# Kernel tuning notes

Hardware: AMD Instinct MI355X
Metric: run time of the kernel (lower is better)

Reference implementation:

```python
import jax, jax.numpy as jnp
import numpy as np

N = 4096      # batch size (PK-sampled)
D = 1024      # feature dim
K = 4         # instances per identity
NUM_IDS = N // K


def setup_inputs() -> dict:
    key = jax.random.key(0)
    inputs = jax.random.normal(key, (N, D), dtype=jnp.float32)
    # PK-structured labels: NUM_IDS identities, K instances each.
    targets = jnp.repeat(jnp.arange(NUM_IDS, dtype=jnp.int32), K)
    # Flags alternate within each identity -> every (same/diff id) x (same/diff flag)
    # combination is non-empty for every anchor row.
    flags = jnp.tile(jnp.array([0, 1, 0, 1], dtype=jnp.int32), N // 4)
    epoch = 10  # unused by the loss, kept for signature fidelity
    return {"inputs": inputs, "targets": targets, "flags": flags, "epoch": epoch}


def reference(inputs, targets, flags, epoch):
    # Pairwise Euclidean distances: ||a||^2 + ||b||^2 - 2 a.b, clamped + sqrt.
    sq = jnp.sum(inputs * inputs, axis=1, keepdims=True)          # [n,1]
    dist = sq + sq.T - 2.0 * (inputs @ inputs.T)                   # [n,n]
    dist = jnp.sqrt(jnp.clip(dist, 1e-12, None))

    same_id = targets[:, None] == targets[None, :]                 # mask_1
    same_fl = flags[:, None] == flags[None, :]                     # mask_2
    m_same_hp = same_id & same_fl
    m_same_hn = (~same_id) & same_fl
    m_dif_hp = same_id & (~same_fl)
    m_dif_hn = (~same_id) & (~same_fl)

    NEG = jnp.asarray(-jnp.inf, dist.dtype)
    POS = jnp.asarray(jnp.inf, dist.dtype)
    dist_same_ap = jnp.max(jnp.where(m_same_hp, dist, NEG), axis=1)
    dist_same_an = jnp.min(jnp.where(m_same_hn, dist, POS), axis=1)
    dist_dif_ap = jnp.max(jnp.where(m_dif_hp, dist, NEG), axis=1)
    dist_dif_an = jnp.min(jnp.where(m_dif_hn, dist, POS), axis=1)

    # torch: first index in the FULL row equal to the masked min (exact equality)
    same_min_idx = jnp.argmax(dist == dist_same_an[:, None], axis=1)  # [n]
    dif_min_idx = jnp.argmax(dist == dist_dif_an[:, None], axis=1)    # [n]
    dist_dif_neg = dist[same_min_idx, dif_min_idx]                    # [n]

    relu = jax.nn.relu
    # MarginRankingLoss(x1, x2, y=1) = mean(relu(x2 - x1 + margin))
    loss_same = jnp.mean(relu(dist_same_ap - dist_same_an + 0.8))
    loss_dif = jnp.mean(relu(dist_dif_ap - dist_dif_an + 0.5))
    loss_neg = jnp.mean(relu(dist_same_ap - dist_dif_neg + 0.3))
    return loss_same + loss_dif + loss_neg
```

## Files before the change

### kernel.cpp

```cpp
#include <hip/hip_runtime.h>

#define NROWS 4096
#define DIM   1024

using f32x4 = __attribute__((ext_vector_type(4))) float;
using bfrag = __attribute__((ext_vector_type(8))) short;

__device__ __forceinline__ unsigned short f2bf(float f) {
  unsigned u = __float_as_uint(f);
  u += 0x7fffu + ((u >> 16) & 1u);
  return (unsigned short)(u >> 16);
}
__device__ __forceinline__ float bf2f(unsigned short b) {
  return __uint_as_float(((unsigned)b) << 16);
}
__device__ __forceinline__ unsigned long long shflx64(unsigned long long v, int m) {
  int lo = __shfl_xor((int)(unsigned)(v & 0xffffffffull), m);
  int hi = __shfl_xor((int)(unsigned)(v >> 32), m);
  return ((unsigned long long)(unsigned)hi << 32) | (unsigned)lo;
}

__global__ void init_kernel(int* maxS, int* maxD, unsigned long long* minS,
                            unsigned long long* minD, float* out) {
  int i = blockIdx.x * 256 + threadIdx.x;
  if (i < NROWS) { maxS[i] = 0; maxD[i] = 0; minS[i] = ~0ull; minD[i] = ~0ull; }
  if (i == 0) out[0] = 0.f;
}

__global__ void prep_kernel(const float* __restrict__ X, unsigned short* __restrict__ Xb,
                            float* __restrict__ sqv) {
  int row = blockIdx.x, t = threadIdx.x;
  float4 v = reinterpret_cast<const float4*>(X + (size_t)row * DIM)[t];
  unsigned short b0 = f2bf(v.x), b1 = f2bf(v.y), b2 = f2bf(v.z), b3 = f2bf(v.w);
  float f0 = bf2f(b0), f1 = bf2f(b1), f2 = bf2f(b2), f3 = bf2f(b3);
  float s = f0 * f0 + f1 * f1 + f2 * f2 + f3 * f3;
  reinterpret_cast<ushort4*>(Xb + (size_t)row * DIM)[t] = make_ushort4(b0, b1, b2, b3);
  for (int m = 32; m; m >>= 1) s += __shfl_xor(s, m);
  __shared__ float ws4[4];
  if ((t & 63) == 0) ws4[t >> 6] = s;
  __syncthreads();
  if (t == 0) sqv[row] = (ws4[0] + ws4[1]) + (ws4[2] + ws4[3]);
}

__global__ __launch_bounds__(256) void gram_kernel(
    const unsigned short* __restrict__ Xb, const float* __restrict__ sqv,
    const int* __restrict__ tg, const int* __restrict__ fl,
    int* maxS, int* maxD, unsigned long long* minS, unsigned long long* minD) {
  __shared__ __attribute__((aligned(16))) char smem[128 * 133 * 4];
  __shared__ float srow[128], scol[128];
  __shared__ int rtg[128], rfl[128], ctg[128], cfl[128];

  int tm = 0, g = blockIdx.x, rem = 32;
  while (g >= rem) { g -= rem; rem--; tm++; }
  int tn = tm + g;
  const int row0 = tm * 128, col0 = tn * 128;
  const int tid = threadIdx.x;
  const int wave = tid >> 6, lane = tid & 63;

  if (tid < 128) {
    srow[tid] = sqv[row0 + tid]; rtg[tid] = tg[row0 + tid]; rfl[tid] = fl[row0 + tid];
  } else {
    int c = tid - 128;
    scol[c] = sqv[col0 + c]; ctg[c] = tg[col0 + c]; cfl[c] = fl[col0 + c];
  }

  unsigned short (*As)[64] = (unsigned short (*)[64])smem;
  unsigned short (*Bs)[64] = (unsigned short (*)[64])(smem + 16384);
  float (*Ds)[133] = (float (*)[133])smem;

  f32x4 acc[4][4] = {};
  const int wr = (wave >> 1) * 64, wc = (wave & 1) * 64;
  const int ksrc = ((lane & 7) ^ (lane >> 3)) * 8;

  for (int ks = 0; ks < DIM; ks += 64) {
    __syncthreads();
#pragma unroll
    for (int q = 0; q < 4; ++q) {
      int base = (wave * 4 + q) * 1024;
      int r = (base >> 7) + (lane >> 3);
      const unsigned short* srcA = Xb + (size_t)(row0 + r) * DIM + ks + ksrc;
      __builtin_amdgcn_global_load_lds(
          (const __attribute__((address_space(1))) void*)srcA,
          (__attribute__((address_space(3))) void*)(smem + base), 16, 0, 0);
      const unsigned short* srcB = Xb + (size_t)(col0 + r) * DIM + ks + ksrc;
      __builtin_amdgcn_global_load_lds(
          (const __attribute__((address_space(1))) void*)srcB,
          (__attribute__((address_space(3))) void*)(smem + 16384 + base), 16, 0, 0);
    }
    __syncthreads();
#pragma unroll
    for (int kk = 0; kk < 2; ++kk) {
      bfrag a[4], b[4];
      int kel = ((kk * 4 + (lane >> 4)) ^ (lane & 7)) * 8;
#pragma unroll
      for (int m = 0; m < 4; ++m)
        a[m] = *(const bfrag*)&As[wr + m * 16 + (lane & 15)][kel];
#pragma unroll
      for (int n = 0; n < 4; ++n)
        b[n] = *(const bfrag*)&Bs[wc + n * 16 + (lane & 15)][kel];
#pragma unroll
      for (int m = 0; m < 4; ++m)
#pragma unroll
        for (int n = 0; n < 4; ++n)
          acc[m][n] = __builtin_amdgcn_mfma_f32_16x16x32_bf16(a[m], b[n], acc[m][n], 0, 0, 0);
    }
  }
  __syncthreads();

#pragma unroll
  for (int m = 0; m < 4; ++m)
#pragma unroll
    for (int n = 0; n < 4; ++n)
#pragma unroll
      for (int r = 0; r < 4; ++r) {
        int lr = wr + m * 16 + (lane >> 4) * 4 + r;
        int lc = wc + n * 16 + (lane & 15);
        float dsq = srow[lr] + scol[lc] - 2.0f * acc[m][n][r];
        Ds[lr][lc] = sqrtf(fmaxf(dsq, 1e-12f));
      }
  __syncthreads();

  {
    int r = tid >> 1, h = tid & 1;
    int ti = rtg[r], fi = rfl[r];
    float mxS = -1.f, mxD = -1.f;
    unsigned long long mnS = ~0ull, mnD = ~0ull;
    for (int c0 = 0; c0 < 64; ++c0) {
      int c = h * 64 + c0;
      float d = Ds[r][c];
      unsigned long long pk =
          ((unsigned long long)__float_as_uint(d) << 32) | (unsigned)(col0 + c);
      bool sid = (ctg[c] == ti), sfl = (cfl[c] == fi);
      if (sid) { if (sfl) mxS = fmaxf(mxS, d); else mxD = fmaxf(mxD, d); }
      else     { if (sfl) { if (pk < mnS) mnS = pk; } else { if (pk < mnD) mnD = pk; } }
    }
    mxS = fmaxf(mxS, __shfl_xor(mxS, 1));
    mxD = fmaxf(mxD, __shfl_xor(mxD, 1));
    unsigned long long o = shflx64(mnS, 1); if (o < mnS) mnS = o;
    o = shflx64(mnD, 1); if (o < mnD) mnD = o;
    if (h == 0) {
      atomicMax(&maxS[row0 + r], __float_as_int(mxS));
      atomicMax(&maxD[row0 + r], __float_as_int(mxD));
      atomicMin(&minS[row0 + r], mnS);
      atomicMin(&minD[row0 + r], mnD);
    }
  }
  {
    int cc = tid >> 1, h = tid & 1;
    int tj = ctg[cc], fj = cfl[cc];
    float mxS = -1.f, mxD = -1.f;
    unsigned long long mnS = ~0ull, mnD = ~0ull;
    for (int r0 = 0; r0 < 64; ++r0) {
      int rr = h * 64 + r0;
      float d = Ds[rr][cc];
      unsigned long long pk =
          ((unsigned long long)__float_as_uint(d) << 32) | (unsigned)(row0 + rr);
      bool sid = (rtg[rr] == tj), sfl = (rfl[rr] == fj);
      if (sid) { if (sfl) mxS = fmaxf(mxS, d); else mxD = fmaxf(mxD, d); }
      else     { if (sfl) { if (pk < mnS) mnS = pk; } else { if (pk < mnD) mnD = pk; } }
    }
    mxS = fmaxf(mxS, __shfl_xor(mxS, 1));
    mxD = fmaxf(mxD, __shfl_xor(mxD, 1));
    unsigned long long o = shflx64(mnS, 1); if (o < mnS) mnS = o;
    o = shflx64(mnD, 1); if (o < mnD) mnD = o;
    if (h == 0) {
      atomicMax(&maxS[col0 + cc], __float_as_int(mxS));
      atomicMax(&maxD[col0 + cc], __float_as_int(mxD));
      atomicMin(&minS[col0 + cc], mnS);
      atomicMin(&minD[col0 + cc], mnD);
    }
  }
}

__global__ void finish_kernel(const unsigned short* __restrict__ Xb,
                              const float* __restrict__ sqv,
                              const int* __restrict__ maxS, const int* __restrict__ maxD,
                              const unsigned long long* __restrict__ minS,
                              const unsigned long long* __restrict__ minD, float* out) {
  int wave = threadIdx.x >> 6, lane = threadIdx.x & 63;
  float part = 0.f;
  for (int rr = 0; rr < 8; ++rr) {
    int row = blockIdx.x * 32 + wave * 8 + rr;
    unsigned long long pS = minS[row], pD = minD[row];
    int ia = (int)(pS & 0xffffffffull);
    int ib = (int)(pD & 0xffffffffull);
    const ushort4* pa = (const ushort4*)(Xb + (size_t)ia * DIM);
    const ushort4* pb = (const ushort4*)(Xb + (size_t)ib * DIM);
    float s = 0.f;
#pragma unroll
    for (int q = 0; q < 4; ++q) {
      ushort4 a = pa[lane + q * 64], b = pb[lane + q * 64];
      s += bf2f(a.x) * bf2f(b.x) + bf2f(a.y) * bf2f(b.y) +
           bf2f(a.z) * bf2f(b.z) + bf2f(a.w) * bf2f(b.w);
    }
    for (int m = 32; m; m >>= 1) s += __shfl_xor(s, m);
    if (lane == 0) {
      float dneg = sqrtf(fmaxf(sqv[ia] + sqv[ib] - 2.f * s, 1e-12f));
      float mS = __int_as_float(maxS[row]);
      float mD = __int_as_float(maxD[row]);
      float mnSv = __uint_as_float((unsigned)(pS >> 32));
      float mnDv = __uint_as_float((unsigned)(pD >> 32));
      part += fmaxf(mS - mnSv + 0.8f, 0.f) + fmaxf(mD - mnDv + 0.5f, 0.f) +
              fmaxf(mS - dneg + 0.3f, 0.f);
    }
  }
  __shared__ float wp[4];
  if (lane == 0) wp[wave] = part;
  __syncthreads();
  if (threadIdx.x == 0)
    atomicAdd(out, ((wp[0] + wp[1]) + (wp[2] + wp[3])) * (1.0f / 4096.0f));
}

extern "C" void kernel_launch(void* const* d_in, const int* in_sizes, int n_in,
                              void* d_out, int out_size, void* d_ws, size_t ws_size,
                              hipStream_t stream) {
  const float* X = (const float*)d_in[0];
  const int* tg  = (const int*)d_in[1];
  const int* fl  = (const int*)d_in[2];
  float* out = (float*)d_out;

  char* w = (char*)d_ws;
  unsigned short* Xb = (unsigned short*)(w);
  float* sqv = (float*)(w + 8388608);
  int* maxS  = (int*)(w + 8404992);
  int* maxD  = (int*)(w + 8421376);
  unsigned long long* minS = (unsigned long long*)(w + 8437760);
  unsigned long long* minD = (unsigned long long*)(w + 8470528);

  init_kernel<<<16, 256, 0, stream>>>(maxS, maxD, minS, minD, out);
  prep_kernel<<<NROWS, 256, 0, stream>>>(X, Xb, sqv);
  gram_kernel<<<528, 256, 0, stream>>>(Xb, sqv, tg, fl, maxS, maxD, minS, minD);
  finish_kernel<<<128, 256, 0, stream>>>(Xb, sqv, maxS, maxD, minS, minD, out);
}
```

Measured before the change: 153.7 us.

## Fuse column reductions into MFMA epilogue and shrink LDS tile for occupancy

The init kernel is folded into prep_kernel, so one launch disappears. In gram_kernel, the column-wise max/min reductions are now done straight from the MFMA accumulators in registers and combined with cross-lane shuffles, instead of being re-read from a full 128x133 LDS distance tile. Row reductions now work on two 64-row halves in a 32KB XOR-swizzled LDS buffer, and identity and flag are packed into a single tag. The smaller LDS footprint plus launch_bounds(256,4) are meant to raise occupancy, at the cost of extra syncs and more register pressure.

```diff
diff --git a/kernel.cpp b/kernel.cpp
--- a/kernel.cpp
+++ b/kernel.cpp
@@ -20,15 +20,10 @@
   return ((unsigned long long)(unsigned)hi << 32) | (unsigned)lo;
 }
 
-__global__ void init_kernel(int* maxS, int* maxD, unsigned long long* minS,
-                            unsigned long long* minD, float* out) {
-  int i = blockIdx.x * 256 + threadIdx.x;
-  if (i < NROWS) { maxS[i] = 0; maxD[i] = 0; minS[i] = ~0ull; minD[i] = ~0ull; }
-  if (i == 0) out[0] = 0.f;
-}
-
 __global__ void prep_kernel(const float* __restrict__ X, unsigned short* __restrict__ Xb,
-                            float* __restrict__ sqv) {
+                            float* __restrict__ sqv, int* maxS, int* maxD,
+                            unsigned long long* minS, unsigned long long* minD,
+                            float* out) {
   int row = blockIdx.x, t = threadIdx.x;
   float4 v = reinterpret_cast<const float4*>(X + (size_t)row * DIM)[t];
   unsigned short b0 = f2bf(v.x), b1 = f2bf(v.y), b2 = f2bf(v.z), b3 = f2bf(v.w);
@@ -39,16 +34,20 @@
   __shared__ float ws4[4];
   if ((t & 63) == 0) ws4[t >> 6] = s;
   __syncthreads();
-  if (t == 0) sqv[row] = (ws4[0] + ws4[1]) + (ws4[2] + ws4[3]);
-}
-
-__global__ __launch_bounds__(256) void gram_kernel(
+  if (t == 0) {
+    sqv[row] = (ws4[0] + ws4[1]) + (ws4[2] + ws4[3]);
+    maxS[row] = 0; maxD[row] = 0; minS[row] = ~0ull; minD[row] = ~0ull;
+    if (row == 0) out[0] = 0.f;
+  }
+}
+
+__global__ __launch_bounds__(256, 4) void gram_kernel(
     const unsigned short* __restrict__ Xb, const float* __restrict__ sqv,
     const int* __restrict__ tg, const int* __restrict__ fl,
     int* maxS, int* maxD, unsigned long long* minS, unsigned long long* minD) {
-  __shared__ __attribute__((aligned(16))) char smem[128 * 133 * 4];
+  __shared__ __attribute__((aligned(16))) char smem[32768];
   __shared__ float srow[128], scol[128];
-  __shared__ int rtg[128], rfl[128], ctg[128], cfl[128];
+  __shared__ int rtagp[128], ctagp[128];
 
   int tm = 0, g = blockIdx.x, rem = 32;
   while (g >= rem) { g -= rem; rem--; tm++; }
@@ -56,17 +55,20 @@
   const int row0 = tm * 128, col0 = tn * 128;
   const int tid = threadIdx.x;
   const int wave = tid >> 6, lane = tid & 63;
+  const int q = lane >> 4, li = lane & 15;
 
   if (tid < 128) {
-    srow[tid] = sqv[row0 + tid]; rtg[tid] = tg[row0 + tid]; rfl[tid] = fl[row0 + tid];
+    srow[tid] = sqv[row0 + tid];
+    rtagp[tid] = (fl[row0 + tid] << 12) | tg[row0 + tid];
   } else {
     int c = tid - 128;
-    scol[c] = sqv[col0 + c]; ctg[c] = tg[col0 + c]; cfl[c] = fl[col0 + c];
+    scol[c] = sqv[col0 + c];
+    ctagp[c] = (fl[col0 + c] << 12) | tg[col0 + c];
   }
 
   unsigned short (*As)[64] = (unsigned short (*)[64])smem;
   unsigned short (*Bs)[64] = (unsigned short (*)[64])(smem + 16384);
-  float (*Ds)[133] = (float (*)[133])smem;
+  float* Ds = (float*)smem;
 
   f32x4 acc[4][4] = {};
   const int wr = (wave >> 1) * 64, wc = (wave & 1) * 64;
@@ -75,8 +77,8 @@
   for (int ks = 0; ks < DIM; ks += 64) {
     __syncthreads();
 #pragma unroll
-    for (int q = 0; q < 4; ++q) {
-      int base = (wave * 4 + q) * 1024;
+    for (int qq = 0; qq < 4; ++qq) {
+      int base = (wave * 4 + qq) * 1024;
       int r = (base >> 7) + (lane >> 3);
       const unsigned short* srcA = Xb + (size_t)(row0 + r) * DIM + ks + ksrc;
       __builtin_amdgcn_global_load_lds(
@@ -91,13 +93,13 @@
 #pragma unroll
     for (int kk = 0; kk < 2; ++kk) {
       bfrag a[4], b[4];
-      int kel = ((kk * 4 + (lane >> 4)) ^ (lane & 7)) * 8;
+      int kel = ((kk * 4 + q) ^ (lane & 7)) * 8;
 #pragma unroll
       for (int m = 0; m < 4; ++m)
-        a[m] = *(const bfrag*)&As[wr + m * 16 + (lane & 15)][kel];
+        a[m] = *(const bfrag*)&As[wr + m * 16 + li][kel];
 #pragma unroll
       for (int n = 0; n < 4; ++n)
-        b[n] = *(const bfrag*)&Bs[wc + n * 16 + (lane & 15)][kel];
+        b[n] = *(const bfrag*)&Bs[wc + n * 16 + li][kel];
 #pragma unroll
       for (int m = 0; m < 4; ++m)
 #pragma unroll
@@ -107,67 +109,89 @@
   }
   __syncthreads();
 
-#pragma unroll
-  for (int m = 0; m < 4; ++m)
-#pragma unroll
-    for (int n = 0; n < 4; ++n)
-#pragma unroll
-      for (int r = 0; r < 4; ++r) {
-        int lr = wr + m * 16 + (lane >> 4) * 4 + r;
-        int lc = wc + n * 16 + (lane & 15);
-        float dsq = srow[lr] + scol[lc] - 2.0f * acc[m][n][r];
-        Ds[lr][lc] = sqrtf(fmaxf(dsq, 1e-12f));
+  float cmxS[4], cmxD[4];
+  unsigned long long cmnS[4], cmnD[4];
+#pragma unroll
+  for (int n = 0; n < 4; ++n) { cmxS[n] = -1.f; cmxD[n] = -1.f; cmnS[n] = ~0ull; cmnD[n] = ~0ull; }
+  int ctv[4]; float scv[4];
+#pragma unroll
+  for (int n = 0; n < 4; ++n) { int lc = wc + n * 16 + li; ctv[n] = ctagp[lc]; scv[n] = scol[lc]; }
+
+#pragma unroll
+  for (int h = 0; h < 2; ++h) {
+    if ((wave >> 1) == h) {
+#pragma unroll
+      for (int m = 0; m < 4; ++m)
+#pragma unroll
+        for (int r = 0; r < 4; ++r) {
+          int lr = wr + m * 16 + q * 4 + r;
+          int rl = lr & 63;
+          int rt = rtagp[lr];
+          float sr = srow[lr];
+          unsigned long long rbase = (unsigned)(row0 + lr);
+#pragma unroll
+          for (int n = 0; n < 4; ++n) {
+            float d = sqrtf(fmaxf(sr + scv[n] - 2.0f * acc[m][n][r], 1e-12f));
+            Ds[rl * 128 + ((wc + n * 16 + li) ^ (lr & 31))] = d;
+            int x = rt ^ ctv[n];
+            unsigned long long pk = ((unsigned long long)__float_as_uint(d) << 32) | rbase;
+            if ((x & 0xFFF) == 0) {
+              if ((x >> 12) == 0) cmxS[n] = fmaxf(cmxS[n], d);
+              else                cmxD[n] = fmaxf(cmxD[n], d);
+            } else {
+              if ((x >> 12) == 0) { if (pk < cmnS[n]) cmnS[n] = pk; }
+              else                { if (pk < cmnD[n]) cmnD[n] = pk; }
+            }
+          }
+        }
+    }
+    __syncthreads();
+    {
+      int rl = (wave & 1) * 32 + (lane & 31);
+      int j = (wave >> 1) * 2 + (lane >> 5);
+      int rt = rtagp[h * 64 + rl];
+      float mxS = -1.f, mxD = -1.f;
+      unsigned long long mnS = ~0ull, mnD = ~0ull;
+      for (int i = 0; i < 32; ++i) {
+        int c = j * 32 + i;
+        float d = Ds[rl * 128 + (c ^ (rl & 31))];
+        int x = rt ^ ctagp[c];
+        unsigned long long pk =
+            ((unsigned long long)__float_as_uint(d) << 32) | (unsigned)(col0 + c);
+        if ((x & 0xFFF) == 0) { if ((x >> 12) == 0) mxS = fmaxf(mxS, d); else mxD = fmaxf(mxD, d); }
+        else { if ((x >> 12) == 0) { if (pk < mnS) mnS = pk; } else { if (pk < mnD) mnD = pk; } }
       }
-  __syncthreads();
-
-  {
-    int r = tid >> 1, h = tid & 1;
-    int ti = rtg[r], fi = rfl[r];
-    float mxS = -1.f, mxD = -1.f;
-    unsigned long long mnS = ~0ull, mnD = ~0ull;
-    for (int c0 = 0; c0 < 64; ++c0) {
-      int c = h * 64 + c0;
-      float d = Ds[r][c];
-      unsigned long long pk =
-          ((unsigned long long)__float_as_uint(d) << 32) | (unsigned)(col0 + c);
-      bool sid = (ctg[c] == ti), sfl = (cfl[c] == fi);
-      if (sid) { if (sfl) mxS = fmaxf(mxS, d); else mxD = fmaxf(mxD, d); }
-      else     { if (sfl) { if (pk < mnS) mnS = pk; } else { if (pk < mnD) mnD = pk; } }
-    }
-    mxS = fmaxf(mxS, __shfl_xor(mxS, 1));
-    mxD = fmaxf(mxD, __shfl_xor(mxD, 1));
-    unsigned long long o = shflx64(mnS, 1); if (o < mnS) mnS = o;
-    o = shflx64(mnD, 1); if (o < mnD) mnD = o;
-    if (h == 0) {
-      atomicMax(&maxS[row0 + r], __float_as_int(mxS));
-      atomicMax(&maxD[row0 + r], __float_as_int(mxD));
-      atomicMin(&minS[row0 + r], mnS);
-      atomicMin(&minD[row0 + r], mnD);
-    }
-  }
-  {
-    int cc = tid >> 1, h = tid & 1;
-    int tj = ctg[cc], fj = cfl[cc];
-    float mxS = -1.f, mxD = -1.f;
-    unsigned long long mnS = ~0ull, mnD = ~0ull;
-    for (int r0 = 0; r0 < 64; ++r0) {
-      int rr = h * 64 + r0;
-      float d = Ds[rr][cc];
-      unsigned long long pk =
-          ((unsigned long long)__float_as_uint(d) << 32) | (unsigned)(row0 + rr);
-      bool sid = (rtg[rr] == tj), sfl = (rfl[rr] == fj);
-      if (sid) { if (sfl) mxS = fmaxf(mxS, d); else mxD = fmaxf(mxD, d); }
-      else     { if (sfl) { if (pk < mnS) mnS = pk; } else { if (pk < mnD) mnD = pk; } }
-    }
-    mxS = fmaxf(mxS, __shfl_xor(mxS, 1));
-    mxD = fmaxf(mxD, __shfl_xor(mxD, 1));
-    unsigned long long o = shflx64(mnS, 1); if (o < mnS) mnS = o;
-    o = shflx64(mnD, 1); if (o < mnD) mnD = o;
-    if (h == 0) {
-      atomicMax(&maxS[col0 + cc], __float_as_int(mxS));
-      atomicMax(&maxD[col0 + cc], __float_as_int(mxD));
-      atomicMin(&minS[col0 + cc], mnS);
-      atomicMin(&minD[col0 + cc], mnD);
+      mxS = fmaxf(mxS, __shfl_xor(mxS, 32));
+      mxD = fmaxf(mxD, __shfl_xor(mxD, 32));
+      unsigned long long o = shflx64(mnS, 32); if (o < mnS) mnS = o;
+      o = shflx64(mnD, 32); if (o < mnD) mnD = o;
+      if (lane < 32) {
+        int gr = row0 + h * 64 + rl;
+        atomicMax(&maxS[gr], __float_as_int(mxS));
+        atomicMax(&maxD[gr], __float_as_int(mxD));
+        atomicMin(&minS[gr], mnS);
+        atomicMin(&minD[gr], mnD);
+      }
+    }
+    __syncthreads();
+  }
+
+#pragma unroll
+  for (int n = 0; n < 4; ++n) {
+    cmxS[n] = fmaxf(cmxS[n], __shfl_xor(cmxS[n], 16));
+    cmxD[n] = fmaxf(cmxD[n], __shfl_xor(cmxD[n], 16));
+    unsigned long long o = shflx64(cmnS[n], 16); if (o < cmnS[n]) cmnS[n] = o;
+    o = shflx64(cmnD[n], 16); if (o < cmnD[n]) cmnD[n] = o;
+    cmxS[n] = fmaxf(cmxS[n], __shfl_xor(cmxS[n], 32));
+    cmxD[n] = fmaxf(cmxD[n], __shfl_xor(cmxD[n], 32));
+    o = shflx64(cmnS[n], 32); if (o < cmnS[n]) cmnS[n] = o;
+    o = shflx64(cmnD[n], 32); if (o < cmnD[n]) cmnD[n] = o;
+    if (lane < 16) {
+      int gc = col0 + wc + n * 16 + lane;
+      atomicMax(&maxS[gc], __float_as_int(cmxS[n]));
+      atomicMax(&maxD[gc], __float_as_int(cmxD[n]));
+      atomicMin(&minS[gc], cmnS[n]);
+      atomicMin(&minD[gc], cmnD[n]);
     }
   }
 }
@@ -188,8 +212,8 @@
     const ushort4* pb = (const ushort4*)(Xb + (size_t)ib * DIM);
     float s = 0.f;
 #pragma unroll
-    for (int q = 0; q < 4; ++q) {
-      ushort4 a = pa[lane + q * 64], b = pb[lane + q * 64];
+    for (int qq = 0; qq < 4; ++qq) {
+      ushort4 a = pa[lane + qq * 64], b = pb[lane + qq * 64];
       s += bf2f(a.x) * bf2f(b.x) + bf2f(a.y) * bf2f(b.y) +
            bf2f(a.z) * bf2f(b.z) + bf2f(a.w) * bf2f(b.w);
     }
@@ -227,8 +251,7 @@
   unsigned long long* minS = (unsigned long long*)(w + 8437760);
   unsigned long long* minD = (unsigned long long*)(w + 8470528);
 
-  init_kernel<<<16, 256, 0, stream>>>(maxS, maxD, minS, minD, out);
-  prep_kernel<<<NROWS, 256, 0, stream>>>(X, Xb, sqv);
+  prep_kernel<<<NROWS, 256, 0, stream>>>(X, Xb, sqv, maxS, maxD, minS, minD, out);
   gram_kernel<<<528, 256, 0, stream>>>(Xb, sqv, tg, fl, maxS, maxD, minS, minD);
   finish_kernel<<<128, 256, 0, stream>>>(Xb, sqv, maxS, maxD, minS, minD, out);
 }
```

After: 165.9 us. 7.9% more time.
